# Optimization experiments

Hardware: AMD Instinct MI355X
Metric: run time of the kernel (lower is better)

## Reference

```python
import jax, jax.numpy as jnp
import numpy as np

N_NODES = 100000
N_EDGES = 1600000
IN_CH = 128
OUT_CH = 16
HEADS = 4
HID = HEADS * OUT_CH  # 64
OUT_SIZE = 4
NEG_SLOPE = 0.2


def _xavier(key, shape, fan_in, fan_out):
    bound = float(np.sqrt(6.0 / (fan_in + fan_out)))
    return jax.random.uniform(key, shape, jnp.float32, -bound, bound)


def setup_inputs() -> dict:
    key = jax.random.key(0)
    ks = jax.random.split(key, 32)
    inp = {
        "x": jax.random.normal(ks[0], (N_NODES, IN_CH), jnp.float32),
        "edge_index": jax.random.randint(ks[1], (2, N_EDGES), 0, N_NODES, jnp.int64),
    }
    cin = IN_CH
    for l in range(4):
        inp[f"W{l}"] = _xavier(ks[2 + 3 * l], (HID, cin), cin, HID)
        inp[f"b{l}"] = jnp.zeros((HID,), jnp.float32)
        inp[f"a{l}"] = _xavier(ks[3 + 3 * l], (HEADS, 2 * OUT_CH), 2 * OUT_CH, 1)
        cin = HID
    inp["fcW"] = _xavier(ks[20], (OUT_SIZE, HID), HID, OUT_SIZE)
    inp["fcb"] = jnp.zeros((OUT_SIZE,), jnp.float32)
    return inp


def _gat_layer(x, src, dst, W, b, att):
    n = x.shape[0]
    h = (x @ W.T + b).reshape(n, HEADS, OUT_CH)  # [N,H,C]
    # cat([x_i,x_j]) . att == (x_i . att[:, :C]) + (x_j . att[:, C:])
    si = jnp.einsum("nhc,hc->nh", h, att[:, :OUT_CH])  # target part
    sj = jnp.einsum("nhc,hc->nh", h, att[:, OUT_CH:])  # source part
    alpha = jax.nn.leaky_relu(si[dst] + sj[src], NEG_SLOPE)  # [E,H]
    deg = jax.ops.segment_sum(jnp.ones((src.shape[0],), x.dtype), dst, num_segments=n)
    alpha = alpha / deg[dst][:, None]
    msg = h[src] * alpha[:, :, None]  # [E,H,C]
    out = jax.ops.segment_sum(msg, dst, num_segments=n)  # [N,H,C]
    return out.reshape(n, HID)


def reference(x, edge_index, W0, b0, a0, W1, b1, a1, W2, b2, a2, W3, b3, a3, fcW, fcb):
    src = edge_index[0]  # x_j
    dst = edge_index[1]  # x_i (aggregation targets)
    for W, b, a in ((W0, b0, a0), (W1, b1, a1), (W2, b2, a2), (W3, b3, a3)):
        x = _gat_layer(x, src, dst, W, b, a)
    return x @ fcW.T + fcb
```

## Files before the change

kernel.cpp:

```cpp
#include <hip/hip_runtime.h>

#define NNODES 100000
#define NEDGES 1600000
#define IN_CH 128
#define HID 64
#define HEADS 4
#define OUT_CH 16
#define OUT_SIZE 4
#define NEG_SLOPE 0.2f
#define NXCD 8
#define CAP 64
#define CAP_SHIFT 6

__global__ __launch_bounds__(256) void k_slot_fill_part(const int* __restrict__ src,
                           const int* __restrict__ dst, int* __restrict__ cursor,
                           int* __restrict__ slots, int E, int rng) {
    const int range = blockIdx.x & (NXCD - 1);
    const int chunk = blockIdx.x >> 3;
    const int lo = range * rng, hi = lo + rng;
    const int base = chunk * 2048 + threadIdx.x;
    #pragma unroll
    for (int i = 0; i < 8; ++i) {
        int e = base + i * 256;
        if (e < E) {
            int d = dst[e];
            if (d >= lo && d < hi) {
                int pos = atomicAdd(&cursor[d], 1);
                if (pos < CAP) slots[((size_t)d << CAP_SHIFT) + pos] = src[e];
            }
        }
    }
}

template<int IN>
__global__ __launch_bounds__(256, 4) void k_linear_t(const float* __restrict__ x,
                         const float* __restrict__ W, const float* __restrict__ bias,
                         const float* __restrict__ att,
                         float* __restrict__ h, float* __restrict__ si, float* __restrict__ sj,
                         int n) {
    constexpr int BM = 64, BK = 64;
    constexpr int LDK = BK + 16;
    constexpr int LDB = HID + 4;
    __shared__ float As[BM][LDK];
    __shared__ float Bs[BK][LDB];

    const int tid = threadIdx.x;
    const int node0 = blockIdx.x * BM;
    const int g = tid >> 4;
    const int v = tid & 15;
    const int tn = v * 4;

    float acc[4][4] = {};
    float4 ra[4], rb[4];

    #pragma unroll
    for (int i = 0; i < 4; ++i) {
        int m = g + 16 * i;
        int gm = node0 + m;
        ra[i] = make_float4(0.f, 0.f, 0.f, 0.f);
        if (gm < n) ra[i] = *reinterpret_cast<const float4*>(&x[(size_t)gm * IN + tn]);
        rb[i] = *reinterpret_cast<const float4*>(&W[(size_t)m * IN + tn]);
    }

    #pragma unroll
    for (int kk = 0; kk < IN; kk += BK) {
        #pragma unroll
        for (int i = 0; i < 4; ++i) {
            int m = g + 16 * i;
            *reinterpret_cast<float4*>(&As[m][tn]) = ra[i];
            Bs[tn + 0][m] = rb[i].x; Bs[tn + 1][m] = rb[i].y;
            Bs[tn + 2][m] = rb[i].z; Bs[tn + 3][m] = rb[i].w;
        }
        __syncthreads();
        if (kk + BK < IN) {
            #pragma unroll
            for (int i = 0; i < 4; ++i) {
                int m = g + 16 * i;
                int gm = node0 + m;
                ra[i] = make_float4(0.f, 0.f, 0.f, 0.f);
                if (gm < n)
                    ra[i] = *reinterpret_cast<const float4*>(&x[(size_t)gm * IN + kk + BK + tn]);
                rb[i] = *reinterpret_cast<const float4*>(&W[(size_t)m * IN + kk + BK + tn]);
            }
        }
        #pragma unroll
        for (int k4 = 0; k4 < BK; k4 += 4) {
            float4 b0 = *reinterpret_cast<const float4*>(&Bs[k4 + 0][tn]);
            float4 b1 = *reinterpret_cast<const float4*>(&Bs[k4 + 1][tn]);
            float4 b2 = *reinterpret_cast<const float4*>(&Bs[k4 + 2][tn]);
            float4 b3 = *reinterpret_cast<const float4*>(&Bs[k4 + 3][tn]);
            #pragma unroll
            for (int r = 0; r < 4; ++r) {
                float4 a = *reinterpret_cast<const float4*>(&As[g + 16 * r][k4]);
                acc[r][0] = fmaf(a.x, b0.x, acc[r][0]);
                acc[r][1] = fmaf(a.x, b0.y, acc[r][1]);
                acc[r][2] = fmaf(a.x, b0.z, acc[r][2]);
                acc[r][3] = fmaf(a.x, b0.w, acc[r][3]);
                acc[r][0] = fmaf(a.y, b1.x, acc[r][0]);
                acc[r][1] = fmaf(a.y, b1.y, acc[r][1]);
                acc[r][2] = fmaf(a.y, b1.z, acc[r][2]);
                acc[r][3] = fmaf(a.y, b1.w, acc[r][3]);
                acc[r][0] = fmaf(a.z, b2.x, acc[r][0]);
                acc[r][1] = fmaf(a.z, b2.y, acc[r][1]);
                acc[r][2] = fmaf(a.z, b2.z, acc[r][2]);
                acc[r][3] = fmaf(a.z, b2.w, acc[r][3]);
                acc[r][0] = fmaf(a.w, b3.x, acc[r][0]);
                acc[r][1] = fmaf(a.w, b3.y, acc[r][1]);
                acc[r][2] = fmaf(a.w, b3.z, acc[r][2]);
                acc[r][3] = fmaf(a.w, b3.w, acc[r][3]);
            }
        }
        __syncthreads();
    }

    float4 bb = *reinterpret_cast<const float4*>(&bias[tn]);
    #pragma unroll
    for (int r = 0; r < 4; ++r) {
        acc[r][0] += bb.x; acc[r][1] += bb.y; acc[r][2] += bb.z; acc[r][3] += bb.w;
        int gm = node0 + g + 16 * r;
        if (gm < n)
            *reinterpret_cast<float4*>(&h[(size_t)gm * HID + tn]) =
                make_float4(acc[r][0], acc[r][1], acc[r][2], acc[r][3]);
    }

    const int head = v >> 2;
    const int cl = (v & 3) * 4;
    const float* arow = att + head * (2 * OUT_CH);
    float pi[4], pj[4];
    #pragma unroll
    for (int r = 0; r < 4; ++r) {
        float vi = 0.f, vj = 0.f;
        #pragma unroll
        for (int c = 0; c < 4; ++c) {
            vi = fmaf(acc[r][c], arow[cl + c], vi);
            vj = fmaf(acc[r][c], arow[OUT_CH + cl + c], vj);
        }
        pi[r] = vi + __shfl_xor(vi, 1); pi[r] += __shfl_xor(pi[r], 2);
        pj[r] = vj + __shfl_xor(vj, 1); pj[r] += __shfl_xor(pj[r], 2);
    }
    {
        int r = v & 3;
        int gm = node0 + g + 16 * r;
        if (gm < n) {
            float siv = (r == 0) ? pi[0] : (r == 1) ? pi[1] : (r == 2) ? pi[2] : pi[3];
            float sjv = (r == 0) ? pj[0] : (r == 1) ? pj[1] : (r == 2) ? pj[2] : pj[3];
            si[gm * HEADS + head] = siv;
            sj[gm * HEADS + head] = sjv;
        }
    }
}

__global__ __launch_bounds__(256) void k_gather_lin(const int* __restrict__ slots,
                        const int* __restrict__ deg,
                        const float* __restrict__ h, const float* __restrict__ si,
                        const float* __restrict__ sj,
                        const float* __restrict__ Wn, const float* __restrict__ bn,
                        const float* __restrict__ attn,
                        float* __restrict__ h_out, float* __restrict__ si_out,
                        float* __restrict__ sj_out, int n) {
    __shared__ float Ws[HID][HID + 1];
    __shared__ float orow[16][HID + 4];

    const int tid  = threadIdx.x;
    const int lane = tid & 63;
    const int l16  = lane & 15;
    const int head = l16 >> 2;
    const int grp  = tid >> 4;
    const int node = blockIdx.x * 16 + grp;
    const bool active = node < n;

    #pragma unroll
    for (int i = 0; i < 4; ++i) {
        int f = tid + i * 256;
        int c = f >> 4;
        int k4 = (f & 15) * 4;
        float4 w = *reinterpret_cast<const float4*>(&Wn[(size_t)c * HID + k4]);
        Ws[k4 + 0][c] = w.x; Ws[k4 + 1][c] = w.y;
        Ws[k4 + 2][c] = w.z; Ws[k4 + 3][c] = w.w;
    }
    __syncthreads();

    int beg = 0, end = 0;
    float sid = 0.f, invd = 0.f;
    if (active) {
        int dg = deg[node];
        beg = node << CAP_SHIFT;
        end = beg + (dg < CAP ? dg : CAP);
        sid = si[node * HEADS + head];
        if (dg > 0) invd = 1.0f / (float)dg;
    }

    float4 acc = make_float4(0.f, 0.f, 0.f, 0.f);
    int j = beg;
    while (j < end) {
        float a[8];
        float4 hv[8];
        #pragma unroll
        for (int u = 0; u < 8; ++u) {
            bool p = (j + u) < end;
            int jj = p ? j + u : beg;
            int s = slots[jj];
            float e = sj[s * HEADS + head];
            hv[u] = *reinterpret_cast<const float4*>(&h[(size_t)s * HID + (l16 << 2)]);
            float av = sid + e;
            av = (av > 0.f) ? av : av * NEG_SLOPE;
            a[u] = p ? av : 0.f;
        }
        #pragma unroll
        for (int u = 0; u < 8; ++u) {
            acc.x = fmaf(hv[u].x, a[u], acc.x);
            acc.y = fmaf(hv[u].y, a[u], acc.y);
            acc.z = fmaf(hv[u].z, a[u], acc.z);
            acc.w = fmaf(hv[u].w, a[u], acc.w);
        }
        j += 8;
    }

    if (active) {
        acc.x *= invd; acc.y *= invd; acc.z *= invd; acc.w *= invd;
        *reinterpret_cast<float4*>(&orow[grp][l16 << 2]) = acc;

        const int c0 = l16 << 2;
        float4 hb = *reinterpret_cast<const float4*>(&bn[c0]);
        float h0 = hb.x, h1 = hb.y, h2 = hb.z, h3 = hb.w;
        #pragma unroll
        for (int k = 0; k < HID; ++k) {
            float o = orow[grp][k];
            float4 w = *reinterpret_cast<const float4*>(&Ws[k][c0]);
            h0 = fmaf(o, w.x, h0);
            h1 = fmaf(o, w.y, h1);
            h2 = fmaf(o, w.z, h2);
            h3 = fmaf(o, w.w, h3);
        }
        *reinterpret_cast<float4*>(&h_out[(size_t)node * HID + c0]) =
            make_float4(h0, h1, h2, h3);

        const int cl = (l16 & 3) * 4;
        const float* arow = attn + head * (2 * OUT_CH);
        float hv4[4] = {h0, h1, h2, h3};
        float vi = 0.f, vj = 0.f;
        #pragma unroll
        for (int c = 0; c < 4; ++c) {
            vi = fmaf(hv4[c], arow[cl + c], vi);
            vj = fmaf(hv4[c], arow[OUT_CH + cl + c], vj);
        }
        vi += __shfl_xor(vi, 1); vi += __shfl_xor(vi, 2);
        vj += __shfl_xor(vj, 1); vj += __shfl_xor(vj, 2);
        if ((l16 & 3) == 0) {
            si_out[node * HEADS + head] = vi;
            sj_out[node * HEADS + head] = vj;
        }
    }
}

__global__ __launch_bounds__(256) void k_gather_fc(const int* __restrict__ slots,
                        const int* __restrict__ deg,
                        const float* __restrict__ h, const float* __restrict__ si,
                        const float* __restrict__ sj,
                        const float* __restrict__ fcW, const float* __restrict__ fcb,
                        float* __restrict__ dout, int n) {
    const int lane = threadIdx.x & 63;
    const int l16  = lane & 15;
    const int head = l16 >> 2;
    const int node = blockIdx.x * 16 + (threadIdx.x >> 4);
    const bool active = node < n;

    int beg = 0, end = 0;
    float sid = 0.f, invd = 0.f;
    if (active) {
        int dg = deg[node];
        beg = node << CAP_SHIFT;
        end = beg + (dg < CAP ? dg : CAP);
        sid = si[node * HEADS + head];
        if (dg > 0) invd = 1.0f / (float)dg;
    }

    float4 acc = make_float4(0.f, 0.f, 0.f, 0.f);
    int j = beg;
    while (j < end) {
        float a[8];
        float4 hv[8];
        #pragma unroll
        for (int u = 0; u < 8; ++u) {
            bool p = (j + u) < end;
            int jj = p ? j + u : beg;
            int s = slots[jj];
            float e = sj[s * HEADS + head];
            hv[u] = *reinterpret_cast<const float4*>(&h[(size_t)s * HID + (l16 << 2)]);
            float av = sid + e;
            av = (av > 0.f) ? av : av * NEG_SLOPE;
            a[u] = p ? av : 0.f;
        }
        #pragma unroll
        for (int u = 0; u < 8; ++u) {
            acc.x = fmaf(hv[u].x, a[u], acc.x);
            acc.y = fmaf(hv[u].y, a[u], acc.y);
            acc.z = fmaf(hv[u].z, a[u], acc.z);
            acc.w = fmaf(hv[u].w, a[u], acc.w);
        }
        j += 8;
    }
    if (active) {
        acc.x *= invd; acc.y *= invd; acc.z *= invd; acc.w *= invd;
        const int c0 = l16 << 2;
        float po[OUT_SIZE];
        #pragma unroll
        for (int o = 0; o < OUT_SIZE; ++o) {
            const float* wr = fcW + o * HID + c0;
            float p = acc.x * wr[0];
            p = fmaf(acc.y, wr[1], p);
            p = fmaf(acc.z, wr[2], p);
            p = fmaf(acc.w, wr[3], p);
            p += __shfl_xor(p, 1);
            p += __shfl_xor(p, 2);
            p += __shfl_xor(p, 4);
            p += __shfl_xor(p, 8);
            po[o] = p;
        }
        if (l16 < OUT_SIZE) {
            float val = (l16 == 0) ? po[0] : (l16 == 1) ? po[1]
                      : (l16 == 2) ? po[2] : po[3];
            dout[(size_t)node * OUT_SIZE + l16] = val + fcb[l16];
        }
    }
}

extern "C" void kernel_launch(void* const* d_in, const int* in_sizes, int n_in,
                              void* d_out, int out_size, void* d_ws, size_t ws_size,
                              hipStream_t stream) {
    const float* x0   = (const float*)d_in[0];
    const int*   ei   = (const int*)d_in[1];
    const int E = in_sizes[1] / 2;
    const int N = in_sizes[0] / IN_CH;
    const int* srcp = ei;
    const int* dstp = ei + E;

    const float* W[4] = {(const float*)d_in[2], (const float*)d_in[5], (const float*)d_in[8],  (const float*)d_in[11]};
    const float* B[4] = {(const float*)d_in[3], (const float*)d_in[6], (const float*)d_in[9],  (const float*)d_in[12]};
    const float* A[4] = {(const float*)d_in[4], (const float*)d_in[7], (const float*)d_in[10], (const float*)d_in[13]};
    const float* fcW = (const float*)d_in[14];
    const float* fcb = (const float*)d_in[15];

    float* ws    = (float*)d_ws;
    float* hA    = ws;
    float* hB    = hA  + (size_t)N * HID;
    float* siA   = hB  + (size_t)N * HID;
    float* sjA   = siA + (size_t)N * HEADS;
    float* siB   = sjA + (size_t)N * HEADS;
    float* sjB   = siB + (size_t)N * HEADS;
    int*   cursor= (int*)(sjB + (size_t)N * HEADS);
    int*   slots = cursor + N;

    const int rng = (N + NXCD - 1) / NXCD;
    hipMemsetAsync(cursor, 0, (size_t)N * sizeof(int), stream);
    const int nchunk = (E + 2047) / 2048;
    k_slot_fill_part<<<nchunk * NXCD, 256, 0, stream>>>(srcp, dstp, cursor, slots, E, rng);

    const int nblk = (N + 63) / 64;
    const int gblk = (N + 15) / 16;

    k_linear_t<IN_CH><<<nblk, 256, 0, stream>>>(x0, W[0], B[0], A[0], hA, siA, sjA, N);
    k_gather_lin<<<gblk, 256, 0, stream>>>(slots, cursor, hA, siA, sjA,
                                           W[1], B[1], A[1], hB, siB, sjB, N);
    k_gather_lin<<<gblk, 256, 0, stream>>>(slots, cursor, hB, siB, sjB,
                                           W[2], B[2], A[2], hA, siA, sjA, N);
    k_gather_lin<<<gblk, 256, 0, stream>>>(slots, cursor, hA, siA, sjA,
                                           W[3], B[3], A[3], hB, siB, sjB, N);
    k_gather_fc<<<gblk, 256, 0, stream>>>(slots, cursor, hB, siB, sjB,
                                          fcW, fcb, (float*)d_out, N);
}
```

Baseline: 417.6 us.

## Fuse edge slot fill and first-layer linear into one interleaved kernel

The edge-bucketing kernel and the first GAT layer's dense linear transform are merged into one launch. Blocks are interleaved in groups of 40, with 32 slot-fill blocks and 8 linear blocks per group, so the atomic-heavy scatter and the compute-bound GEMM run at the same time on the GPU. This removes one launch and its serialization. In exchange, the slot-fill blocks now inherit the linear path's shared-memory footprint and the launch_bounds(256,4) occupancy limit, which may reduce how many scatter blocks can be resident at once.

```diff
diff --git a/kernel.cpp b/kernel.cpp
--- a/kernel.cpp
+++ b/kernel.cpp
@@ -12,32 +12,41 @@
 #define CAP 64
 #define CAP_SHIFT 6
 
-__global__ __launch_bounds__(256) void k_slot_fill_part(const int* __restrict__ src,
-                           const int* __restrict__ dst, int* __restrict__ cursor,
-                           int* __restrict__ slots, int E, int rng) {
-    const int range = blockIdx.x & (NXCD - 1);
-    const int chunk = blockIdx.x >> 3;
-    const int lo = range * rng, hi = lo + rng;
-    const int base = chunk * 2048 + threadIdx.x;
-    #pragma unroll
-    for (int i = 0; i < 8; ++i) {
-        int e = base + i * 256;
-        if (e < E) {
-            int d = dst[e];
-            if (d >= lo && d < hi) {
-                int pos = atomicAdd(&cursor[d], 1);
-                if (pos < CAP) slots[((size_t)d << CAP_SHIFT) + pos] = src[e];
+__global__ __launch_bounds__(256, 4) void k_prep(
+        const int* __restrict__ src, const int* __restrict__ dst,
+        int* __restrict__ cursor, int* __restrict__ slots, int E, int rng, int nslot,
+        const float* __restrict__ x, const float* __restrict__ W,
+        const float* __restrict__ bias, const float* __restrict__ att,
+        float* __restrict__ h, float* __restrict__ si, float* __restrict__ sj,
+        int nlin, int n) {
+    const int grp40 = blockIdx.x / 40;
+    const int r40   = blockIdx.x % 40;
+
+    if (r40 < 32) {
+        const int slotId = grp40 * 32 + r40;
+        if (slotId >= nslot) return;
+        const int range = slotId & (NXCD - 1);
+        const int chunk = slotId >> 3;
+        const int lo = range * rng, hi = lo + rng;
+        const int base = chunk * 2048 + threadIdx.x;
+        #pragma unroll
+        for (int i = 0; i < 8; ++i) {
+            int e = base + i * 256;
+            if (e < E) {
+                int d = dst[e];
+                if (d >= lo && d < hi) {
+                    int pos = atomicAdd(&cursor[d], 1);
+                    if (pos < CAP) slots[((size_t)d << CAP_SHIFT) + pos] = src[e];
+                }
             }
         }
-    }
-}
-
-template<int IN>
-__global__ __launch_bounds__(256, 4) void k_linear_t(const float* __restrict__ x,
-                         const float* __restrict__ W, const float* __restrict__ bias,
-                         const float* __restrict__ att,
-                         float* __restrict__ h, float* __restrict__ si, float* __restrict__ sj,
-                         int n) {
+        return;
+    }
+
+    const int linId = grp40 * 8 + (r40 - 32);
+    if (linId >= nlin) return;
+
+    constexpr int IN = IN_CH;
     constexpr int BM = 64, BK = 64;
     constexpr int LDK = BK + 16;
     constexpr int LDB = HID + 4;
@@ -45,7 +54,7 @@
     __shared__ float Bs[BK][LDB];
 
     const int tid = threadIdx.x;
-    const int node0 = blockIdx.x * BM;
+    const int node0 = linId * BM;
     const int g = tid >> 4;
     const int v = tid & 15;
     const int tn = v * 4;
@@ -353,13 +362,16 @@
 
     const int rng = (N + NXCD - 1) / NXCD;
     hipMemsetAsync(cursor, 0, (size_t)N * sizeof(int), stream);
+
     const int nchunk = (E + 2047) / 2048;
-    k_slot_fill_part<<<nchunk * NXCD, 256, 0, stream>>>(srcp, dstp, cursor, slots, E, rng);
-
-    const int nblk = (N + 63) / 64;
+    const int nslot  = nchunk * NXCD;
+    const int nlin   = (N + 63) / 64;
+    const int ngroups = ((nslot + 31) / 32 > (nlin + 7) / 8) ? (nslot + 31) / 32
+                                                             : (nlin + 7) / 8;
+    k_prep<<<ngroups * 40, 256, 0, stream>>>(srcp, dstp, cursor, slots, E, rng, nslot,
+                                             x0, W[0], B[0], A[0], hA, siA, sjA, nlin, N);
+
     const int gblk = (N + 15) / 16;
-
-    k_linear_t<IN_CH><<<nblk, 256, 0, stream>>>(x0, W[0], B[0], A[0], hA, siA, sjA, N);
     k_gather_lin<<<gblk, 256, 0, stream>>>(slots, cursor, hA, siA, sjA,
                                            W[1], B[1], A[1], hB, siB, sjB, N);
     k_gather_lin<<<gblk, 256, 0, stream>>>(slots, cursor, hB, siB, sjB,
```

New measurement: 386.6 us. -7.4%, faster.
